# Performance work log

Hardware: AMD Instinct MI355X
Metric: run time of the kernel (lower is better)

## Reference

```python
import jax, jax.numpy as jnp
import numpy as np

N_AGENTS = 512
HID = 256
OBS = 128


def setup_inputs() -> dict:
    key = jax.random.key(0)
    ks = jax.random.split(key, 10)
    s = 0.02  # weight init scale
    f32 = jnp.float32
    return {
        "inputs": jax.random.normal(ks[0], (N_AGENTS, OBS), f32),
        "fc1_w": jax.random.normal(ks[1], (HID, OBS), f32) * s,
        "fc1_b": jnp.zeros((HID,), f32),
        "in_proj_w": jax.random.normal(ks[2], (3 * HID, HID), f32) * s,
        "in_proj_b": jnp.zeros((3 * HID,), f32),
        "out_proj_w": jax.random.normal(ks[3], (HID, HID), f32) * s,
        "out_proj_b": jnp.zeros((HID,), f32),
        "fc2_w": jax.random.normal(ks[4], (HID, 2 * HID), f32) * s,
        "fc2_b": jnp.zeros((HID,), f32),
        "fc3_w": jax.random.normal(ks[5], (2, HID), f32) * s,
        "fc3_b": jnp.zeros((2,), f32),
        "vfc2_w": jax.random.normal(ks[6], (HID, HID * N_AGENTS), f32) * s,
        "vfc2_b": jnp.zeros((HID,), f32),
        "vfc3_w": jax.random.normal(ks[7], (1, HID), f32) * s,
        "vfc3_b": jnp.zeros((1,), f32),
    }


def reference(inputs, fc1_w, fc1_b, in_proj_w, in_proj_b, out_proj_w, out_proj_b,
              fc2_w, fc2_b, fc3_w, fc3_b, vfc2_w, vfc2_b, vfc3_w, vfc3_b):
    n = inputs.shape[0]
    d = fc1_w.shape[0]
    # per-agent embed
    hid = jax.nn.relu(inputs @ fc1_w.T + fc1_b)                 # [n, d]
    # single-head self-attention (torch MultiheadAttention, 1 head)
    qkv = hid @ in_proj_w.T + in_proj_b                         # [n, 3d]
    q, k, v = jnp.split(qkv, 3, axis=-1)
    scores = (q @ k.T) / jnp.sqrt(jnp.asarray(d, hid.dtype))    # [n, n]
    attn = jax.nn.softmax(scores, axis=-1)
    h = (attn @ v) @ out_proj_w.T + out_proj_b                  # [n, d]
    # all-pairs edge features restricted to strict upper triangle
    iu0, iu1 = jnp.triu_indices(n, 1)                           # P = n(n-1)/2
    pairs = jnp.concatenate([h[iu0], h[iu1]], axis=1)           # [P, 2d]
    x = jax.nn.relu(pairs @ fc2_w.T + fc2_b)                    # [P, d]
    action_out = jax.nn.softmax(x @ fc3_w.T + fc3_b, axis=-1)   # [P, 2]
    # value head over flattened node embeddings
    vh = jax.nn.relu(hid.reshape(1, -1) @ vfc2_w.T + vfc2_b)    # [1, d]
    value = vh @ vfc3_w.T + vfc3_b                              # [1, 1]
    value = jnp.broadcast_to(value, (action_out.shape[0], 1))   # [P, 1]
    return jnp.concatenate([action_out, value], axis=1)         # [P, 3]
```

## Files before the change

### kernel.cpp

```cpp
#include <hip/hip_runtime.h>
#include <math.h>

#define N_AG   512
#define HIDD   256
#define OBSD   128

__device__ __forceinline__ void fma4(float4& acc, float4 a, float4 b){
    acc.x += a.x*b.x; acc.y += a.y*b.y; acc.z += a.z*b.z; acc.w += a.w*b.w;
}
__device__ __forceinline__ float hsum(float4 a){ return (a.x+a.y)+(a.z+a.w); }

__global__ __launch_bounds__(256, 2) void k_fc1(const float* __restrict__ in,
        const float* __restrict__ w, const float* __restrict__ b,
        float* __restrict__ hid){
    __shared__ float lin[8*OBSD];
    int at = blockIdx.y, ot = blockIdx.x, t = threadIdx.x;
    ((float4*)lin)[t] = ((const float4*)(in + at*8*OBSD))[t];
    __syncthreads();
    int ol = t & 63, g = t >> 6;
    int o = ot*64 + ol;
    const float4* w4 = (const float4*)(w + o*OBSD);
    const float4* la = (const float4*)(lin + (g*2)*OBSD);
    const float4* lb = (const float4*)(lin + (g*2+1)*OBSD);
    float4 a0 = {0,0,0,0}, a1 = {0,0,0,0};
    #pragma unroll
    for (int c = 0; c < OBSD/4; ++c){
        float4 wv = w4[c];
        fma4(a0, la[c], wv);
        fma4(a1, lb[c], wv);
    }
    float bb = b[o];
    int ag = at*8 + g*2;
    hid[ag*HIDD + o]     = fmaxf(hsum(a0) + bb, 0.f);
    hid[(ag+1)*HIDD + o] = fmaxf(hsum(a1) + bb, 0.f);
}

__global__ __launch_bounds__(256, 2) void k_qkv(const float* __restrict__ hid,
        const float* __restrict__ w, const float* __restrict__ b,
        float* __restrict__ qkv){
    __shared__ float lin[8*HIDD];
    int at = blockIdx.y, ot = blockIdx.x, t = threadIdx.x;
    const float4* in4 = (const float4*)(hid + at*8*HIDD);
    ((float4*)lin)[t]       = in4[t];
    ((float4*)lin)[t + 256] = in4[t + 256];
    __syncthreads();
    int ol = t & 63, g = t >> 6;
    int o = ot*64 + ol;
    const float4* w4 = (const float4*)(w + o*HIDD);
    const float4* la = (const float4*)(lin + (g*2)*HIDD);
    const float4* lb = (const float4*)(lin + (g*2+1)*HIDD);
    float4 a0 = {0,0,0,0}, a1 = {0,0,0,0};
    #pragma unroll 8
    for (int c = 0; c < HIDD/4; ++c){
        float4 wv = w4[c];
        fma4(a0, la[c], wv);
        fma4(a1, lb[c], wv);
    }
    float bb = b[o];
    int ag = at*8 + g*2;
    qkv[ag*768 + o]     = hsum(a0) + bb;
    qkv[(ag+1)*768 + o] = hsum(a1) + bb;
}

__global__ __launch_bounds__(256, 2) void k_attn_vpart(const float* __restrict__ qkv,
        const float* __restrict__ ow, const float* __restrict__ ob,
        const float* __restrict__ hid, const float* __restrict__ vw,
        float* __restrict__ hout, float* __restrict__ partial){
    int t = threadIdx.x;
    if (blockIdx.x >= 128){
        int id = blockIdx.x - 128;
        int chunk = id & 7, o = id >> 3;
        const float4* h4 = (const float4*)hid;
        const float4* w4 = (const float4*)vw;
        long base  = (long)chunk*4096;
        long wbase = (long)o*32768 + base;
        float4 aa = {0,0,0,0}, ab = {0,0,0,0};
        #pragma unroll 4
        for (int it = 0; it < 8; ++it){
            fma4(aa, h4[base + it*256 + t],       w4[wbase + it*256 + t]);
            fma4(ab, h4[base + (it+8)*256 + t],   w4[wbase + (it+8)*256 + t]);
        }
        float acc = hsum(aa) + hsum(ab);
        for (int off = 32; off; off >>= 1) acc += __shfl_xor(acc, off);
        __shared__ float redv[4];
        int lane = t & 63, wid = t >> 6;
        if (lane == 0) redv[wid] = acc;
        __syncthreads();
        if (t == 0) partial[o*8 + chunk] = redv[0]+redv[1]+redv[2]+redv[3];
        return;
    }
    int r0 = blockIdx.x*4;
    __shared__ float qs[4*HIDD];
    __shared__ float sc[4*512];
    __shared__ float av[4*HIDD];
    {
        int r = t >> 6, c4 = t & 63;
        ((float4*)qs)[t] = ((const float4*)(qkv + (r0+r)*768))[c4];
    }
    __syncthreads();
    const float4* q0 = (const float4*)qs;
    const float4* q1 = (const float4*)(qs + HIDD);
    const float4* q2 = (const float4*)(qs + 2*HIDD);
    const float4* q3 = (const float4*)(qs + 3*HIDD);
    #pragma unroll
    for (int jj = 0; jj < 2; ++jj){
        int j = t + jj*256;
        const float4* k4 = (const float4*)(qkv + j*768 + HIDD);
        float4 a0 = {0,0,0,0}, a1 = {0,0,0,0}, a2 = {0,0,0,0}, a3 = {0,0,0,0};
        #pragma unroll 8
        for (int c = 0; c < HIDD/4; ++c){
            float4 kv = k4[c];
            fma4(a0, q0[c], kv);
            fma4(a1, q1[c], kv);
            fma4(a2, q2[c], kv);
            fma4(a3, q3[c], kv);
        }
        sc[j]        = hsum(a0) * 0.0625f;
        sc[512 + j]  = hsum(a1) * 0.0625f;
        sc[1024 + j] = hsum(a2) * 0.0625f;
        sc[1536 + j] = hsum(a3) * 0.0625f;
    }
    __syncthreads();
    {
        int wv = t >> 6, ln = t & 63;
        float* row = sc + wv*512;
        float vals[8];
        float m = -1e30f;
        #pragma unroll
        for (int k = 0; k < 8; ++k){ vals[k] = row[ln + k*64]; m = fmaxf(m, vals[k]); }
        for (int off = 32; off; off >>= 1) m = fmaxf(m, __shfl_xor(m, off));
        float s = 0.f;
        #pragma unroll
        for (int k = 0; k < 8; ++k){ vals[k] = expf(vals[k] - m); s += vals[k]; }
        for (int off = 32; off; off >>= 1) s += __shfl_xor(s, off);
        float inv = 1.f / s;
        #pragma unroll
        for (int k = 0; k < 8; ++k) row[ln + k*64] = vals[k]*inv;
    }
    __syncthreads();
    {
        float4 p = {0,0,0,0};
        #pragma unroll 8
        for (int j = 0; j < 512; ++j){
            float vv = qkv[j*768 + 512 + t];
            p.x += sc[j]*vv;
            p.y += sc[512+j]*vv;
            p.z += sc[1024+j]*vv;
            p.w += sc[1536+j]*vv;
        }
        av[t] = p.x; av[HIDD+t] = p.y; av[2*HIDD+t] = p.z; av[3*HIDD+t] = p.w;
    }
    __syncthreads();
    {
        const float4* w4 = (const float4*)(ow + t*HIDD);
        const float4* a0 = (const float4*)av;
        const float4* a1 = (const float4*)(av + HIDD);
        const float4* a2 = (const float4*)(av + 2*HIDD);
        const float4* a3 = (const float4*)(av + 3*HIDD);
        float4 h0 = {0,0,0,0}, h1 = {0,0,0,0}, h2 = {0,0,0,0}, h3 = {0,0,0,0};
        #pragma unroll 8
        for (int c = 0; c < HIDD/4; ++c){
            float4 wv = w4[c];
            fma4(h0, a0[c], wv);
            fma4(h1, a1[c], wv);
            fma4(h2, a2[c], wv);
            fma4(h3, a3[c], wv);
        }
        float bb = ob[t];
        hout[r0*HIDD + t]       = hsum(h0) + bb;
        hout[(r0+1)*HIDD + t]   = hsum(h1) + bb;
        hout[(r0+2)*HIDD + t]   = hsum(h2) + bb;
        hout[(r0+3)*HIDD + t]   = hsum(h3) + bb;
    }
}

__global__ __launch_bounds__(256, 2) void k_ab_value(const float* __restrict__ hin,
        const float* __restrict__ w2, const float* __restrict__ b2,
        const float* __restrict__ partial, const float* __restrict__ vb,
        const float* __restrict__ v3w, const float* __restrict__ v3b,
        float* __restrict__ A, float* __restrict__ B, float* __restrict__ value){
    int t = threadIdx.x;
    if (blockIdx.x == 512){
        float s = vb[t];
        #pragma unroll
        for (int c = 0; c < 8; ++c) s += partial[t*8 + c];
        s = fmaxf(s, 0.f) * v3w[t];
        for (int off = 32; off; off >>= 1) s += __shfl_xor(s, off);
        __shared__ float redv[4];
        int lane = t & 63, wid = t >> 6;
        if (lane == 0) redv[wid] = s;
        __syncthreads();
        if (t == 0) value[0] = redv[0]+redv[1]+redv[2]+redv[3] + v3b[0];
        return;
    }
    __shared__ float lin[8*HIDD];
    int id = blockIdx.x, at = id >> 3, ot = id & 7;
    const float4* in4 = (const float4*)(hin + at*8*HIDD);
    ((float4*)lin)[t]       = in4[t];
    ((float4*)lin)[t + 256] = in4[t + 256];
    __syncthreads();
    int ol = t & 63, g = t >> 6;
    int o2 = ot*64 + ol;
    bool isA = o2 < HIDD;
    int o = isA ? o2 : o2 - HIDD;
    const float4* w4 = (const float4*)(w2 + o*512 + (isA ? 0 : HIDD));
    const float4* la = (const float4*)(lin + (g*2)*HIDD);
    const float4* lb = (const float4*)(lin + (g*2+1)*HIDD);
    float4 acc0 = {0,0,0,0}, acc1 = {0,0,0,0};
    #pragma unroll 8
    for (int c = 0; c < HIDD/4; ++c){
        float4 wv = w4[c];
        fma4(acc0, la[c], wv);
        fma4(acc1, lb[c], wv);
    }
    int a0 = at*8 + g*2;
    float* dst = isA ? A : B;
    float bb = isA ? b2[o] : 0.f;
    dst[a0*HIDD + o]     = hsum(acc0) + bb;
    dst[(a0+1)*HIDD + o] = hsum(acc1) + bb;
}

__global__ __launch_bounds__(256, 2) void k_pairs(const float* __restrict__ A,
        const float* __restrict__ B, const float* __restrict__ w3,
        const float* __restrict__ b3, const float* __restrict__ value,
        float* __restrict__ out){
    int ti = blockIdx.x, tj = blockIdx.y;
    if (tj < ti) return;
    __shared__ float la[16*260], lb[16*260], lw[256];
    int t = threadIdx.x;
    #pragma unroll
    for (int l = 0; l < 4; ++l){
        int idx = l*256 + t;
        int r = idx >> 6, c4 = idx & 63;
        ((float4*)la)[r*65 + c4] = ((const float4*)A)[(ti*16 + r)*64 + c4];
        ((float4*)lb)[r*65 + c4] = ((const float4*)B)[(tj*16 + r)*64 + c4];
    }
    lw[t] = w3[t] - w3[256 + t];
    __syncthreads();
    float val = value[0];
    float bd  = b3[0] - b3[1];
    int il = t >> 4, jl = t & 15;
    int i = ti*16 + il, j = tj*16 + jl;
    if (j > i){
        const float4* a4 = (const float4*)(la + il*260);
        const float4* b4 = (const float4*)(lb + jl*260);
        const float4* w4 = (const float4*)lw;
        float4 acc = {0,0,0,0};
        #pragma unroll 8
        for (int c = 0; c < 64; ++c){
            float4 aa = a4[c], bb = b4[c], wv = w4[c];
            acc.x += fmaxf(aa.x + bb.x, 0.f)*wv.x;
            acc.y += fmaxf(aa.y + bb.y, 0.f)*wv.y;
            acc.z += fmaxf(aa.z + bb.z, 0.f)*wv.z;
            acc.w += fmaxf(aa.w + bb.w, 0.f)*wv.w;
        }
        float z = hsum(acc) + bd;
        float o0 = 1.f/(1.f + expf(-z));
        int p = i*511 - (i*(i-1))/2 + (j - i - 1);
        out[3*p]   = o0;
        out[3*p+1] = 1.f - o0;
        out[3*p+2] = val;
    }
}

extern "C" void kernel_launch(void* const* d_in, const int* in_sizes, int n_in,
                              void* d_out, int out_size, void* d_ws, size_t ws_size,
                              hipStream_t stream){
    const float* inputs = (const float*)d_in[0];
    const float* fc1_w  = (const float*)d_in[1];
    const float* fc1_b  = (const float*)d_in[2];
    const float* inp_w  = (const float*)d_in[3];
    const float* inp_b  = (const float*)d_in[4];
    const float* outp_w = (const float*)d_in[5];
    const float* outp_b = (const float*)d_in[6];
    const float* fc2_w  = (const float*)d_in[7];
    const float* fc2_b  = (const float*)d_in[8];
    const float* fc3_w  = (const float*)d_in[9];
    const float* fc3_b  = (const float*)d_in[10];
    const float* vfc2_w = (const float*)d_in[11];
    const float* vfc2_b = (const float*)d_in[12];
    const float* vfc3_w = (const float*)d_in[13];
    const float* vfc3_b = (const float*)d_in[14];
    float* out = (float*)d_out;
    float* ws  = (float*)d_ws;
    float* hid     = ws;
    float* qkv     = ws + 131072;
    float* h       = ws + 524288;
    float* A       = ws + 655360;
    float* B       = ws + 786432;
    float* partial = ws + 917504;
    float* value   = ws + 919552;

    k_fc1       <<<dim3(4, 64),  256, 0, stream>>>(inputs, fc1_w, fc1_b, hid);
    k_qkv       <<<dim3(12, 64), 256, 0, stream>>>(hid, inp_w, inp_b, qkv);
    k_attn_vpart<<<dim3(2176),   256, 0, stream>>>(qkv, outp_w, outp_b, hid, vfc2_w, h, partial);
    k_ab_value  <<<dim3(513),    256, 0, stream>>>(h, fc2_w, fc2_b, partial, vfc2_b, vfc3_w, vfc3_b, A, B, value);
    k_pairs     <<<dim3(32, 32), 256, 0, stream>>>(A, B, fc3_w, fc3_b, value, out);
}
```

Baseline: 304.8 us.

## Split fused attention into tiled QK^T, softmax, and P·(V·Wo) GEMM kernels

The per-row fused attention kernel is replaced by register-tiled 64x64 GEMMs with shared-memory staging. It computes QK^T into a global score matrix, runs a separate softmax kernel, precomputes V·Wo by reassociating (PV)Wo, then multiplies P by VW. Tiling is meant to remove the redundant uncoalesced K/V global reads each 4-row block did. The cost is two extra launches and a global round trip of the 512x512 score matrix, and the h kernel has only 32 blocks.

```diff
diff --git a/kernel.cpp b/kernel.cpp
--- a/kernel.cpp
+++ b/kernel.cpp
@@ -9,6 +9,32 @@
     acc.x += a.x*b.x; acc.y += a.y*b.y; acc.z += a.z*b.z; acc.w += a.w*b.w;
 }
 __device__ __forceinline__ float hsum(float4 a){ return (a.x+a.y)+(a.z+a.w); }
+
+__device__ __forceinline__ void stage_rows(float* dst, const float* __restrict__ src,
+        int row0, int stride, int colbase, int t){
+    #pragma unroll
+    for (int half = 0; half < 2; ++half){
+        int idx = half*256 + t;
+        int row = idx >> 3, c4 = idx & 7;
+        float4 v = *(const float4*)(src + (row0+row)*stride + colbase + c4*4);
+        dst[(c4*4+0)*68 + row] = v.x;
+        dst[(c4*4+1)*68 + row] = v.y;
+        dst[(c4*4+2)*68 + row] = v.z;
+        dst[(c4*4+3)*68 + row] = v.w;
+    }
+}
+__device__ __forceinline__ void tile_compute(const float* As, const float* Bs,
+        int tx, int ty, float4 acc[4]){
+    #pragma unroll
+    for (int kk = 0; kk < 32; ++kk){
+        float4 a = *(const float4*)(As + kk*68 + ty*4);
+        float4 b = *(const float4*)(Bs + kk*68 + tx*4);
+        acc[0].x += a.x*b.x; acc[0].y += a.x*b.y; acc[0].z += a.x*b.z; acc[0].w += a.x*b.w;
+        acc[1].x += a.y*b.x; acc[1].y += a.y*b.y; acc[1].z += a.y*b.z; acc[1].w += a.y*b.w;
+        acc[2].x += a.z*b.x; acc[2].y += a.z*b.y; acc[2].z += a.z*b.z; acc[2].w += a.z*b.w;
+        acc[3].x += a.w*b.x; acc[3].y += a.w*b.y; acc[3].z += a.w*b.z; acc[3].w += a.w*b.w;
+    }
+}
 
 __global__ __launch_bounds__(256, 2) void k_fc1(const float* __restrict__ in,
         const float* __restrict__ w, const float* __restrict__ b,
@@ -62,115 +88,119 @@
     qkv[(ag+1)*768 + o] = hsum(a1) + bb;
 }
 
-__global__ __launch_bounds__(256, 2) void k_attn_vpart(const float* __restrict__ qkv,
-        const float* __restrict__ ow, const float* __restrict__ ob,
-        const float* __restrict__ hid, const float* __restrict__ vw,
-        float* __restrict__ hout, float* __restrict__ partial){
+__global__ __launch_bounds__(256, 2) void k_big(const float* __restrict__ qkv,
+        const float* __restrict__ ow, const float* __restrict__ hid,
+        const float* __restrict__ vw_w, float* __restrict__ S,
+        float* __restrict__ VW, float* __restrict__ partial){
+    __shared__ float As[32*68];
+    __shared__ float Bs[32*68];
     int t = threadIdx.x;
-    if (blockIdx.x >= 128){
-        int id = blockIdx.x - 128;
-        int chunk = id & 7, o = id >> 3;
-        const float4* h4 = (const float4*)hid;
-        const float4* w4 = (const float4*)vw;
-        long base  = (long)chunk*4096;
-        long wbase = (long)o*32768 + base;
-        float4 aa = {0,0,0,0}, ab = {0,0,0,0};
-        #pragma unroll 4
-        for (int it = 0; it < 8; ++it){
-            fma4(aa, h4[base + it*256 + t],       w4[wbase + it*256 + t]);
-            fma4(ab, h4[base + (it+8)*256 + t],   w4[wbase + (it+8)*256 + t]);
-        }
-        float acc = hsum(aa) + hsum(ab);
-        for (int off = 32; off; off >>= 1) acc += __shfl_xor(acc, off);
-        __shared__ float redv[4];
-        int lane = t & 63, wid = t >> 6;
-        if (lane == 0) redv[wid] = acc;
+    int bid = blockIdx.x;
+    if (bid < 64){
+        int ti = bid >> 3, tj = bid & 7;
+        int i0 = ti*64, j0 = tj*64;
+        int tx = t & 15, ty = t >> 4;
+        float4 acc[4] = {{0,0,0,0},{0,0,0,0},{0,0,0,0},{0,0,0,0}};
+        for (int k0 = 0; k0 < 256; k0 += 32){
+            __syncthreads();
+            stage_rows(As, qkv, i0, 768, k0,       t);
+            stage_rows(Bs, qkv, j0, 768, 256 + k0, t);
+            __syncthreads();
+            tile_compute(As, Bs, tx, ty, acc);
+        }
+        #pragma unroll
+        for (int r = 0; r < 4; ++r){
+            float4 o;
+            o.x = acc[r].x*0.0625f; o.y = acc[r].y*0.0625f;
+            o.z = acc[r].z*0.0625f; o.w = acc[r].w*0.0625f;
+            *(float4*)(S + (i0+ty*4+r)*512 + j0 + tx*4) = o;
+        }
+        return;
+    }
+    if (bid < 96){
+        int b2 = bid - 64;
+        int ti = b2 >> 2, tj = b2 & 3;
+        int j0 = ti*64, d0 = tj*64;
+        int tx = t & 15, ty = t >> 4;
+        float4 acc[4] = {{0,0,0,0},{0,0,0,0},{0,0,0,0},{0,0,0,0}};
+        for (int k0 = 0; k0 < 256; k0 += 32){
+            __syncthreads();
+            stage_rows(As, qkv, j0, 768, 512 + k0, t);
+            stage_rows(Bs, ow,  d0, 256, k0,       t);
+            __syncthreads();
+            tile_compute(As, Bs, tx, ty, acc);
+        }
+        #pragma unroll
+        for (int r = 0; r < 4; ++r)
+            *(float4*)(VW + (j0+ty*4+r)*256 + d0 + tx*4) = acc[r];
+        return;
+    }
+    int id = bid - 96;
+    int chunk = id & 7, o = id >> 3;
+    const float4* h4 = (const float4*)hid;
+    const float4* w4 = (const float4*)vw_w;
+    long base  = (long)chunk*4096;
+    long wbase = (long)o*32768 + base;
+    float4 aa = {0,0,0,0}, ab = {0,0,0,0};
+    #pragma unroll 4
+    for (int it = 0; it < 8; ++it){
+        fma4(aa, h4[base + it*256 + t],     w4[wbase + it*256 + t]);
+        fma4(ab, h4[base + (it+8)*256 + t], w4[wbase + (it+8)*256 + t]);
+    }
+    float acc = hsum(aa) + hsum(ab);
+    for (int off = 32; off; off >>= 1) acc += __shfl_xor(acc, off);
+    int lane = t & 63, wid = t >> 6;
+    if (lane == 0) As[wid] = acc;
+    __syncthreads();
+    if (t == 0) partial[o*8 + chunk] = As[0]+As[1]+As[2]+As[3];
+}
+
+__global__ __launch_bounds__(256, 2) void k_softmax(float* __restrict__ S){
+    int t = threadIdx.x, w = t >> 6, ln = t & 63;
+    float* row = S + (blockIdx.x*4 + w)*512;
+    float v[8];
+    float m = -1e30f;
+    #pragma unroll
+    for (int k = 0; k < 8; ++k){ v[k] = row[ln + k*64]; m = fmaxf(m, v[k]); }
+    for (int off = 32; off; off >>= 1) m = fmaxf(m, __shfl_xor(m, off));
+    float s = 0.f;
+    #pragma unroll
+    for (int k = 0; k < 8; ++k){ v[k] = expf(v[k] - m); s += v[k]; }
+    for (int off = 32; off; off >>= 1) s += __shfl_xor(s, off);
+    float inv = 1.f / s;
+    #pragma unroll
+    for (int k = 0; k < 8; ++k) row[ln + k*64] = v[k]*inv;
+}
+
+__global__ __launch_bounds__(256, 2) void k_h(const float* __restrict__ P,
+        const float* __restrict__ VW, const float* __restrict__ ob,
+        float* __restrict__ hout){
+    __shared__ float As[32*68];
+    __shared__ float Bs[32*68];
+    int bid = blockIdx.x;
+    int ti = bid >> 2, tj = bid & 3;
+    int i0 = ti*64, d0 = tj*64;
+    int t = threadIdx.x, tx = t & 15, ty = t >> 4;
+    float4 acc[4] = {{0,0,0,0},{0,0,0,0},{0,0,0,0},{0,0,0,0}};
+    for (int k0 = 0; k0 < 512; k0 += 32){
         __syncthreads();
-        if (t == 0) partial[o*8 + chunk] = redv[0]+redv[1]+redv[2]+redv[3];
-        return;
-    }
-    int r0 = blockIdx.x*4;
-    __shared__ float qs[4*HIDD];
-    __shared__ float sc[4*512];
-    __shared__ float av[4*HIDD];
-    {
-        int r = t >> 6, c4 = t & 63;
-        ((float4*)qs)[t] = ((const float4*)(qkv + (r0+r)*768))[c4];
-    }
-    __syncthreads();
-    const float4* q0 = (const float4*)qs;
-    const float4* q1 = (const float4*)(qs + HIDD);
-    const float4* q2 = (const float4*)(qs + 2*HIDD);
-    const float4* q3 = (const float4*)(qs + 3*HIDD);
-    #pragma unroll
-    for (int jj = 0; jj < 2; ++jj){
-        int j = t + jj*256;
-        const float4* k4 = (const float4*)(qkv + j*768 + HIDD);
-        float4 a0 = {0,0,0,0}, a1 = {0,0,0,0}, a2 = {0,0,0,0}, a3 = {0,0,0,0};
-        #pragma unroll 8
-        for (int c = 0; c < HIDD/4; ++c){
-            float4 kv = k4[c];
-            fma4(a0, q0[c], kv);
-            fma4(a1, q1[c], kv);
-            fma4(a2, q2[c], kv);
-            fma4(a3, q3[c], kv);
-        }
-        sc[j]        = hsum(a0) * 0.0625f;
-        sc[512 + j]  = hsum(a1) * 0.0625f;
-        sc[1024 + j] = hsum(a2) * 0.0625f;
-        sc[1536 + j] = hsum(a3) * 0.0625f;
-    }
-    __syncthreads();
-    {
-        int wv = t >> 6, ln = t & 63;
-        float* row = sc + wv*512;
-        float vals[8];
-        float m = -1e30f;
+        stage_rows(As, P, i0, 512, k0, t);
         #pragma unroll
-        for (int k = 0; k < 8; ++k){ vals[k] = row[ln + k*64]; m = fmaxf(m, vals[k]); }
-        for (int off = 32; off; off >>= 1) m = fmaxf(m, __shfl_xor(m, off));
-        float s = 0.f;
-        #pragma unroll
-        for (int k = 0; k < 8; ++k){ vals[k] = expf(vals[k] - m); s += vals[k]; }
-        for (int off = 32; off; off >>= 1) s += __shfl_xor(s, off);
-        float inv = 1.f / s;
-        #pragma unroll
-        for (int k = 0; k < 8; ++k) row[ln + k*64] = vals[k]*inv;
-    }
-    __syncthreads();
-    {
-        float4 p = {0,0,0,0};
-        #pragma unroll 8
-        for (int j = 0; j < 512; ++j){
-            float vv = qkv[j*768 + 512 + t];
-            p.x += sc[j]*vv;
-            p.y += sc[512+j]*vv;
-            p.z += sc[1024+j]*vv;
-            p.w += sc[1536+j]*vv;
-        }
-        av[t] = p.x; av[HIDD+t] = p.y; av[2*HIDD+t] = p.z; av[3*HIDD+t] = p.w;
-    }
-    __syncthreads();
-    {
-        const float4* w4 = (const float4*)(ow + t*HIDD);
-        const float4* a0 = (const float4*)av;
-        const float4* a1 = (const float4*)(av + HIDD);
-        const float4* a2 = (const float4*)(av + 2*HIDD);
-        const float4* a3 = (const float4*)(av + 3*HIDD);
-        float4 h0 = {0,0,0,0}, h1 = {0,0,0,0}, h2 = {0,0,0,0}, h3 = {0,0,0,0};
-        #pragma unroll 8
-        for (int c = 0; c < HIDD/4; ++c){
-            float4 wv = w4[c];
-            fma4(h0, a0[c], wv);
-            fma4(h1, a1[c], wv);
-            fma4(h2, a2[c], wv);
-            fma4(h3, a3[c], wv);
-        }
-        float bb = ob[t];
-        hout[r0*HIDD + t]       = hsum(h0) + bb;
-        hout[(r0+1)*HIDD + t]   = hsum(h1) + bb;
-        hout[(r0+2)*HIDD + t]   = hsum(h2) + bb;
-        hout[(r0+3)*HIDD + t]   = hsum(h3) + bb;
+        for (int half = 0; half < 2; ++half){
+            int idx = half*256 + t;
+            int kkr = idx >> 4, c4 = idx & 15;
+            *(float4*)(Bs + kkr*68 + c4*4) = *(const float4*)(VW + (k0+kkr)*256 + d0 + c4*4);
+        }
+        __syncthreads();
+        tile_compute(As, Bs, tx, ty, acc);
+    }
+    float4 bb = *(const float4*)(ob + d0 + tx*4);
+    #pragma unroll
+    for (int r = 0; r < 4; ++r){
+        float4 o;
+        o.x = acc[r].x + bb.x; o.y = acc[r].y + bb.y;
+        o.z = acc[r].z + bb.z; o.w = acc[r].w + bb.w;
+        *(float4*)(hout + (i0+ty*4+r)*256 + d0 + tx*4) = o;
     }
 }
 
@@ -285,15 +315,19 @@
     float* ws  = (float*)d_ws;
     float* hid     = ws;
     float* qkv     = ws + 131072;
-    float* h       = ws + 524288;
-    float* A       = ws + 655360;
-    float* B       = ws + 786432;
-    float* partial = ws + 917504;
-    float* value   = ws + 919552;
-
-    k_fc1       <<<dim3(4, 64),  256, 0, stream>>>(inputs, fc1_w, fc1_b, hid);
-    k_qkv       <<<dim3(12, 64), 256, 0, stream>>>(hid, inp_w, inp_b, qkv);
-    k_attn_vpart<<<dim3(2176),   256, 0, stream>>>(qkv, outp_w, outp_b, hid, vfc2_w, h, partial);
-    k_ab_value  <<<dim3(513),    256, 0, stream>>>(h, fc2_w, fc2_b, partial, vfc2_b, vfc3_w, vfc3_b, A, B, value);
-    k_pairs     <<<dim3(32, 32), 256, 0, stream>>>(A, B, fc3_w, fc3_b, value, out);
-}
+    float* S       = ws + 524288;
+    float* VW      = ws + 786432;
+    float* h       = ws + 917504;
+    float* A       = ws + 1048576;
+    float* B       = ws + 1179648;
+    float* partial = ws + 1310720;
+    float* value   = ws + 1312768;
+
+    k_fc1     <<<dim3(4, 64),  256, 0, stream>>>(inputs, fc1_w, fc1_b, hid);
+    k_qkv     <<<dim3(12, 64), 256, 0, stream>>>(hid, inp_w, inp_b, qkv);
+    k_big     <<<dim3(2144),   256, 0, stream>>>(qkv, outp_w, hid, vfc2_w, S, VW, partial);
+    k_softmax <<<dim3(128),    256, 0, stream>>>(S);
+    k_h       <<<dim3(32),     256, 0, stream>>>(S, VW, outp_b, h);
+    k_ab_value<<<dim3(513),    256, 0, stream>>>(h, fc2_w, fc2_b, partial, vfc2_b, vfc3_w, vfc3_b, A, B, value);
+    k_pairs   <<<dim3(32, 32), 256, 0, stream>>>(A, B, fc3_w, fc3_b, value, out);
+}
```

Result: no change. 299.3 us (-1.8%).
